# Kernel tuning notes

Hardware: AMD Instinct MI355X
Metric: run time of the kernel (lower is better)

The kernel has to match this reference:

```python
import jax, jax.numpy as jnp
import numpy as np

N_NODES = 50000
N_EDGES = 800000
D_IN = 64
D_OUT = 64


def setup_inputs() -> dict:
    key = jax.random.key(0)
    k1, k2, k3 = jax.random.split(key, 3)
    x = jax.random.normal(k1, (N_NODES, D_IN), dtype=jnp.float32)
    edge_index = jax.random.randint(k2, (2, N_EDGES), 0, N_NODES, dtype=jnp.int64)
    # xavier_uniform for weight [in, out]
    limit = np.sqrt(6.0 / (D_IN + D_OUT)).astype(np.float32)
    weight = jax.random.uniform(k3, (D_IN, D_OUT), dtype=jnp.float32, minval=-limit, maxval=limit)
    bias = jnp.zeros((D_OUT,), dtype=jnp.float32)
    return {"x": x, "edge_index": edge_index, "weight": weight, "bias": bias}


def reference(x, edge_index, weight, bias):
    n = x.shape[0]
    # add self loops
    loops = jnp.arange(n, dtype=edge_index.dtype)
    row = jnp.concatenate([edge_index[0], loops])  # [E+N]
    col = jnp.concatenate([edge_index[1], loops])  # [E+N]
    # degree over row (as in torch_geometric degree(row, N))
    deg = jax.ops.segment_sum(jnp.ones_like(row, dtype=x.dtype), row, num_segments=n)
    deg_inv_sqrt = jnp.where(deg > 0, jax.lax.rsqrt(deg), jnp.zeros_like(deg))
    norm = deg_inv_sqrt[row] * deg_inv_sqrt[col]  # [E+N]
    h = x @ weight  # [N, D_OUT]
    # gather-scale-scatter: out[col] += h[row] * norm
    out = jax.ops.segment_sum(h[row] * norm[:, None], col, num_segments=n)
    return out + bias
```

## Files before the change

kernel.cpp:

```cpp
#include <hip/hip_runtime.h>
#include <hip/hip_bf16.h>


constexpr int N_NODES = 50000;
constexpr int N_EDGES = 800000;
constexpr int D = 64;
constexpr int NB_SCAN = (N_NODES + 255) / 256;

constexpr int B_SLICE = 64;
constexpr int SLICE = N_EDGES / B_SLICE;
constexpr int PACK8 = N_NODES / 4;
constexpr int QUAR = N_NODES / 4;

static __device__ __forceinline__ unsigned short f2bf(float f) {
    unsigned u = __float_as_uint(f);
    unsigned r = (u + 0x7fffu + ((u >> 16) & 1u)) >> 16;
    return (unsigned short)r;
}
static __device__ __forceinline__ float bf2f(unsigned short s) {
    return __uint_as_float((unsigned)s << 16);
}

__global__ __launch_bounds__(1024) void hist_priv_kernel(const int* __restrict__ ei,
                                                         unsigned* __restrict__ bh) {
    __shared__ unsigned loc[PACK8];
    int b = blockIdx.x;
    int s = b & (B_SLICE - 1);
    const int* arr = (b < B_SLICE) ? ei : ei + N_EDGES;
    for (int w = threadIdx.x; w < PACK8; w += 1024) loc[w] = 0;
    __syncthreads();
    const int* p = arr + s * SLICE;
    for (int i = threadIdx.x; i < SLICE; i += 1024) {
        int k = p[i];
        atomicAdd(&loc[k >> 2], 1u << (8 * (k & 3)));
    }
    __syncthreads();
    unsigned* dst = bh + (size_t)b * PACK8;
    for (int w = threadIdx.x; w < PACK8; w += 1024) dst[w] = loc[w];
}

__global__ __launch_bounds__(256) void reduce_scan_kernel(const unsigned* __restrict__ bh,
                                                          float* __restrict__ dis,
                                                          int* __restrict__ offs_local,
                                                          int* __restrict__ partials,
                                                          unsigned char* __restrict__ bs8) {
    int t = threadIdx.x;
    int i = blockIdx.x * 256 + t;
    unsigned cl = 0;
    if (i < N_NODES) {
        const int w = i >> 2;
        const unsigned sh = 8 * (i & 3);
        const unsigned* prow = bh + w;
        unsigned dl = 0;
#pragma unroll
        for (int g = 0; g < 4; ++g) {
            unsigned vr[16];
#pragma unroll
            for (int k = 0; k < 16; ++k) vr[k] = prow[(size_t)(g * 16 + k) * PACK8];
#pragma unroll
            for (int k = 0; k < 16; ++k) dl += (vr[k] >> sh) & 0xffu;
        }
        dis[i] = rsqrtf((float)dl + 1.0f);
        const unsigned* pcol = bh + (size_t)B_SLICE * PACK8 + w;
#pragma unroll
        for (int g = 0; g < 4; ++g) {
            unsigned vr[16];
#pragma unroll
            for (int k = 0; k < 16; ++k) vr[k] = pcol[(size_t)(g * 16 + k) * PACK8];
#pragma unroll
            for (int k = 0; k < 16; ++k) {
                bs8[(size_t)(g * 16 + k) * N_NODES + i] = (unsigned char)cl;
                cl += (vr[k] >> sh) & 0xffu;
            }
        }
    }
    __shared__ int s[256];
    s[t] = (int)cl;
    __syncthreads();
    for (int d = 1; d < 256; d <<= 1) {
        int u = (t >= d) ? s[t - d] : 0;
        __syncthreads();
        s[t] += u;
        __syncthreads();
    }
    if (i < N_NODES) offs_local[i] = s[t] - (int)cl;
    if (t == 255) partials[blockIdx.x] = s[t];
}

__global__ __launch_bounds__(256, 4) void gemm_kernel(const float* __restrict__ x,
                                                      const float* __restrict__ W,
                                                      const float* __restrict__ dis,
                                                      unsigned short* __restrict__ hs) {
    __shared__ float Xs[64][68];
    __shared__ float Ws[64][64];
    int t = threadIdx.x;
    int n0 = blockIdx.x * 64;

    const float4* W4 = (const float4*)W;
    float4* Ws4 = (float4*)Ws;
#pragma unroll
    for (int i = 0; i < 4; ++i) Ws4[t + i * 256] = W4[t + i * 256];

    const float4* x4 = (const float4*)(x + (size_t)n0 * D);
#pragma unroll
    for (int i = 0; i < 4; ++i) {
        int f = t + i * 256;
        int r = f >> 4, c = (f & 15) << 2;
        float4 v = make_float4(0.f, 0.f, 0.f, 0.f);
        if (n0 + r < N_NODES) v = x4[f];
        Xs[r][c] = v.x; Xs[r][c + 1] = v.y; Xs[r][c + 2] = v.z; Xs[r][c + 3] = v.w;
    }
    __syncthreads();

    int tx = t & 15, ty = t >> 4;
    float acc[4][4] = {};
#pragma unroll 8
    for (int k = 0; k < D; ++k) {
        float a[4], bb[4];
#pragma unroll
        for (int i = 0; i < 4; ++i) a[i] = Xs[ty * 4 + i][k];
#pragma unroll
        for (int jj = 0; jj < 4; ++jj) bb[jj] = Ws[k][tx * 4 + jj];
#pragma unroll
        for (int i = 0; i < 4; ++i)
#pragma unroll
            for (int jj = 0; jj < 4; ++jj)
                acc[i][jj] = fmaf(a[i], bb[jj], acc[i][jj]);
    }

#pragma unroll
    for (int i = 0; i < 4; ++i) {
        int r = ty * 4 + i;
        if (n0 + r < N_NODES) {
            float dr = dis[n0 + r];
            ushort4 v;
            v.x = f2bf(acc[i][0] * dr); v.y = f2bf(acc[i][1] * dr);
            v.z = f2bf(acc[i][2] * dr); v.w = f2bf(acc[i][3] * dr);
            *(ushort4*)(hs + (size_t)(n0 + r) * D + tx * 4) = v;
        }
    }
}

__global__ __launch_bounds__(1024) void bucket_det_kernel(const int* __restrict__ ei,
                                                          const int* __restrict__ offs_local,
                                                          const int* __restrict__ partials,
                                                          const unsigned char* __restrict__ bs8,
                                                          int* __restrict__ csr,
                                                          int* __restrict__ offs) {
    __shared__ unsigned pos[QUAR];
    __shared__ int pref[256];
    const int t = threadIdx.x;

    if (t < 256) pref[t] = (t < NB_SCAN) ? partials[t] : 0;
    __syncthreads();
    for (int d = 1; d < 256; d <<= 1) {
        int u = 0;
        if (t < 256 && t >= d) u = pref[t - d];
        __syncthreads();
        if (t < 256) pref[t] += u;
        __syncthreads();
    }
    if (t < 256) {
        int inc = pref[t];
        int own = (t < NB_SCAN) ? partials[t] : 0;
        pref[t] = inc - own;
    }
    __syncthreads();

    const int s = blockIdx.x >> 2;
    const int q = blockIdx.x & 3;
    const int c0 = q * QUAR;
    const int* olq = offs_local + c0;
    const unsigned char* relq = bs8 + (size_t)s * N_NODES + c0;
    const bool write_offs = (s == 0);
    for (int w = t; w < QUAR; w += 1024) {
        int node = c0 + w;
        int off = pref[node >> 8] + olq[w];
        pos[w] = (unsigned)off + relq[w];
        if (write_offs) offs[node] = off;
    }
    if (write_offs && q == 3 && t == 0) offs[N_NODES] = N_EDGES;
    __syncthreads();

    const int* rowp = ei + s * SLICE;
    const int* colp = ei + N_EDGES + s * SLICE;
    for (int i = t; i < SLICE; i += 1024) {
        int c = colp[i];
        if (c >= c0 && c < c0 + QUAR) {
            unsigned p = atomicAdd(&pos[c - c0], 1u);
            csr[p] = rowp[i];
        }
    }
}

__global__ __launch_bounds__(256) void gather_kernel(const int* __restrict__ offs,
                                                     const int* __restrict__ csr,
                                                     const unsigned short* __restrict__ hs,
                                                     const float* __restrict__ dis,
                                                     const float* __restrict__ bias,
                                                     float* __restrict__ out) {
    int wave = threadIdx.x >> 6;
    int j = threadIdx.x & 63;
    int n = blockIdx.x * 4 + wave;
    if (n >= N_NODES) return;

    float a[8];
    a[0] = bf2f(hs[(size_t)n * D + j]);
#pragma unroll
    for (int k = 1; k < 8; ++k) a[k] = 0.f;

    int beg = __builtin_amdgcn_readfirstlane(offs[n]);
    int m   = __builtin_amdgcn_readfirstlane(offs[n + 1]) - beg;
    const int* p = csr + beg;

    int i = 0;
    for (; i + 16 <= m; i += 16) {
        int r[16];
        float v[16];
#pragma unroll
        for (int k = 0; k < 16; ++k) r[k] = p[i + k];
#pragma unroll
        for (int k = 0; k < 16; ++k) v[k] = bf2f(hs[(size_t)r[k] * D + j]);
#pragma unroll
        for (int k = 0; k < 16; ++k) a[k & 7] += v[k];
    }
    for (; i + 4 <= m; i += 4) {
        int r0 = p[i], r1 = p[i + 1], r2 = p[i + 2], r3 = p[i + 3];
        a[0] += bf2f(hs[(size_t)r0 * D + j]);
        a[1] += bf2f(hs[(size_t)r1 * D + j]);
        a[2] += bf2f(hs[(size_t)r2 * D + j]);
        a[3] += bf2f(hs[(size_t)r3 * D + j]);
    }
    for (; i < m; ++i) a[1] += bf2f(hs[(size_t)p[i] * D + j]);
    float tot = ((a[0] + a[1]) + (a[2] + a[3])) + ((a[4] + a[5]) + (a[6] + a[7]));
    out[(size_t)n * D + j] = fmaf(dis[n], tot, bias[j]);
}


__global__ void histf_kernel(const int* __restrict__ row, const int* __restrict__ col,
                             int* __restrict__ degi, int* __restrict__ cnt) {
    int e = blockIdx.x * blockDim.x + threadIdx.x;
    if (e < N_EDGES) {
        atomicAdd(&degi[row[e]], 1);
        atomicAdd(&cnt[col[e]], 1);
    }
}

__global__ void disf_kernel(int* __restrict__ degi) {
    int i = blockIdx.x * blockDim.x + threadIdx.x;
    if (i < N_NODES) {
        float d = (float)degi[i] + 1.0f;
        ((float*)degi)[i] = rsqrtf(d);
    }
}

__global__ void block_scan_kernel(const int* __restrict__ cnt, int* __restrict__ offs,
                                  int* __restrict__ partials) {
    __shared__ int s[256];
    int t = threadIdx.x;
    int i = blockIdx.x * 256 + t;
    int v = (i < N_NODES) ? cnt[i] : 0;
    s[t] = v;
    __syncthreads();
    for (int d = 1; d < 256; d <<= 1) {
        int u = (t >= d) ? s[t - d] : 0;
        __syncthreads();
        s[t] += u;
        __syncthreads();
    }
    if (i < N_NODES) offs[i] = s[t] - v;
    if (t == 255) partials[blockIdx.x] = s[t];
}

__global__ void scan_partials_kernel(int* __restrict__ partials) {
    __shared__ int s[256];
    int t = threadIdx.x;
    int v = (t < NB_SCAN) ? partials[t] : 0;
    s[t] = v;
    __syncthreads();
    for (int d = 1; d < 256; d <<= 1) {
        int u = (t >= d) ? s[t - d] : 0;
        __syncthreads();
        s[t] += u;
        __syncthreads();
    }
    if (t < NB_SCAN) partials[t] = s[t] - v;
}

__global__ void add_off_kernel(int* __restrict__ offs, const int* __restrict__ partials) {
    int i = blockIdx.x * 256 + threadIdx.x;
    if (i < N_NODES) offs[i] += partials[blockIdx.x];
    if (i == 0) offs[N_NODES] = N_EDGES;
}

__global__ void bucket_fb_kernel(const int* __restrict__ row, const int* __restrict__ col,
                                 const int* __restrict__ offs, int* __restrict__ cur,
                                 int* __restrict__ csr) {
    int e = blockIdx.x * blockDim.x + threadIdx.x;
    if (e < N_EDGES) {
        int c = col[e];
        int pos = offs[c] + atomicAdd(&cur[c], 1);
        csr[pos] = row[e];
    }
}


extern "C" void kernel_launch(void* const* d_in, const int* in_sizes, int n_in,
                              void* d_out, int out_size, void* d_ws, size_t ws_size,
                              hipStream_t stream) {
    const float* x    = (const float*)d_in[0];
    const int*   ei   = (const int*)d_in[1];
    const float* W    = (const float*)d_in[2];
    const float* bias = (const float*)d_in[3];
    float* out = (float*)d_out;

    char* ws = (char*)d_ws;
    float*          dis      = (float*)(ws + 0);
    int*            offs     = (int*)(ws + 200000);
    int*            offs_loc = (int*)(ws + 400064);
    int*            cur      = (int*)(ws + 600064);
    int*            partials = (int*)(ws + 800064);
    int*            csr      = (int*)(ws + 801088);
    unsigned short* hs       = (unsigned short*)(ws + 4001088);
    unsigned*       bh       = (unsigned*)(ws + 10401088);
    unsigned char*  bs8      = (unsigned char*)(ws + 16801088);

    const size_t WS_NEEDED = 20001088;

    if (ws_size >= WS_NEEDED) {
        hist_priv_kernel<<<2 * B_SLICE, 1024, 0, stream>>>(ei, bh);
        reduce_scan_kernel<<<NB_SCAN, 256, 0, stream>>>(bh, dis, offs_loc, partials, bs8);
        gemm_kernel<<<(N_NODES + 63) / 64, 256, 0, stream>>>(x, W, dis, hs);
        bucket_det_kernel<<<4 * B_SLICE, 1024, 0, stream>>>(ei, offs_loc, partials, bs8,
                                                            csr, offs);
        gather_kernel<<<(N_NODES + 3) / 4, 256, 0, stream>>>(offs, csr, hs, dis, bias, out);
    } else {
        const int* row = ei;
        const int* col = ei + N_EDGES;
        int* degi = (int*)dis;
        int* cntf = offs_loc;
        hipMemsetAsync(ws, 0, 800064, stream);
        histf_kernel<<<(N_EDGES + 255) / 256, 256, 0, stream>>>(row, col, degi, cntf);
        disf_kernel<<<(N_NODES + 255) / 256, 256, 0, stream>>>(degi);
        block_scan_kernel<<<NB_SCAN, 256, 0, stream>>>(cntf, offs, partials);
        scan_partials_kernel<<<1, 256, 0, stream>>>(partials);
        add_off_kernel<<<NB_SCAN, 256, 0, stream>>>(offs, partials);
        gemm_kernel<<<(N_NODES + 63) / 64, 256, 0, stream>>>(x, W, dis, hs);
        bucket_fb_kernel<<<(N_EDGES + 255) / 256, 256, 0, stream>>>(row, col, offs, cur, csr);
        gather_kernel<<<(N_NODES + 3) / 4, 256, 0, stream>>>(offs, csr, hs, dis, bias, out);
    }
}
```

Baseline: 134.1 us.

## Move offset computation into GEMM and pack bucket cursors as bytes in LDS

The global CSR offset computation (scan of block partials plus local offsets) moves out of every bucket block and into the first blocks of the GEMM kernel, which writes offs to global memory. The bucket kernel then initializes its shared cursors from per-slice byte-relative counts packed four per 32-bit word and uses shifted atomic adds, cutting its LDS footprint by 4x and dropping the redundant per-block scan. Each edge now reads offs[c] from global memory. Correctness relies on per-slice per-node counts staying below 256 so byte counters never overflow into neighbours.

```diff
diff --git a/kernel.cpp b/kernel.cpp
--- a/kernel.cpp
+++ b/kernel.cpp
@@ -90,10 +90,32 @@
 __global__ __launch_bounds__(256, 4) void gemm_kernel(const float* __restrict__ x,
                                                       const float* __restrict__ W,
                                                       const float* __restrict__ dis,
-                                                      unsigned short* __restrict__ hs) {
+                                                      unsigned short* __restrict__ hs,
+                                                      const int* __restrict__ offs_local,
+                                                      const int* __restrict__ partials,
+                                                      int* __restrict__ offs,
+                                                      int do_offs) {
     __shared__ float Xs[64][68];
     __shared__ float Ws[64][64];
+    __shared__ int pref[256];
     int t = threadIdx.x;
+    int b = blockIdx.x;
+
+    if (do_offs && b < NB_SCAN) {
+        pref[t] = (t < NB_SCAN) ? partials[t] : 0;
+        __syncthreads();
+        for (int d = 1; d < 256; d <<= 1) {
+            int u = (t >= d) ? pref[t - d] : 0;
+            __syncthreads();
+            pref[t] += u;
+            __syncthreads();
+        }
+        int base = pref[b] - partials[b];
+        int node = b * 256 + t;
+        if (node < N_NODES) offs[node] = base + offs_local[node];
+        if (b == 0 && t == 0) offs[N_NODES] = N_EDGES;
+    }
+
     int n0 = blockIdx.x * 64;
 
     const float4* W4 = (const float4*)W;
@@ -142,53 +164,29 @@
 }
 
 __global__ __launch_bounds__(1024) void bucket_det_kernel(const int* __restrict__ ei,
-                                                          const int* __restrict__ offs_local,
-                                                          const int* __restrict__ partials,
                                                           const unsigned char* __restrict__ bs8,
-                                                          int* __restrict__ csr,
-                                                          int* __restrict__ offs) {
-    __shared__ unsigned pos[QUAR];
-    __shared__ int pref[256];
+                                                          const int* __restrict__ offs,
+                                                          int* __restrict__ csr) {
+    __shared__ unsigned pos[QUAR / 4];
     const int t = threadIdx.x;
-
-    if (t < 256) pref[t] = (t < NB_SCAN) ? partials[t] : 0;
-    __syncthreads();
-    for (int d = 1; d < 256; d <<= 1) {
-        int u = 0;
-        if (t < 256 && t >= d) u = pref[t - d];
-        __syncthreads();
-        if (t < 256) pref[t] += u;
-        __syncthreads();
-    }
-    if (t < 256) {
-        int inc = pref[t];
-        int own = (t < NB_SCAN) ? partials[t] : 0;
-        pref[t] = inc - own;
-    }
-    __syncthreads();
-
     const int s = blockIdx.x >> 2;
     const int q = blockIdx.x & 3;
     const int c0 = q * QUAR;
-    const int* olq = offs_local + c0;
-    const unsigned char* relq = bs8 + (size_t)s * N_NODES + c0;
-    const bool write_offs = (s == 0);
-    for (int w = t; w < QUAR; w += 1024) {
-        int node = c0 + w;
-        int off = pref[node >> 8] + olq[w];
-        pos[w] = (unsigned)off + relq[w];
-        if (write_offs) offs[node] = off;
-    }
-    if (write_offs && q == 3 && t == 0) offs[N_NODES] = N_EDGES;
+
+    const unsigned* rel32 = (const unsigned*)(bs8 + (size_t)s * N_NODES + c0);
+    for (int w = t; w < QUAR / 4; w += 1024) pos[w] = rel32[w];
     __syncthreads();
 
     const int* rowp = ei + s * SLICE;
     const int* colp = ei + N_EDGES + s * SLICE;
     for (int i = t; i < SLICE; i += 1024) {
         int c = colp[i];
-        if (c >= c0 && c < c0 + QUAR) {
-            unsigned p = atomicAdd(&pos[c - c0], 1u);
-            csr[p] = rowp[i];
+        unsigned cc = (unsigned)(c - c0);
+        if (cc < (unsigned)QUAR) {
+            int base = offs[c];
+            unsigned old = atomicAdd(&pos[cc >> 2], 1u << (8 * (cc & 3)));
+            unsigned rel = (old >> (8 * (cc & 3))) & 0xffu;
+            csr[base + (int)rel] = rowp[i];
         }
     }
 }
@@ -330,9 +328,9 @@
     if (ws_size >= WS_NEEDED) {
         hist_priv_kernel<<<2 * B_SLICE, 1024, 0, stream>>>(ei, bh);
         reduce_scan_kernel<<<NB_SCAN, 256, 0, stream>>>(bh, dis, offs_loc, partials, bs8);
-        gemm_kernel<<<(N_NODES + 63) / 64, 256, 0, stream>>>(x, W, dis, hs);
-        bucket_det_kernel<<<4 * B_SLICE, 1024, 0, stream>>>(ei, offs_loc, partials, bs8,
-                                                            csr, offs);
+        gemm_kernel<<<(N_NODES + 63) / 64, 256, 0, stream>>>(x, W, dis, hs,
+                                                             offs_loc, partials, offs, 1);
+        bucket_det_kernel<<<4 * B_SLICE, 1024, 0, stream>>>(ei, bs8, offs, csr);
         gather_kernel<<<(N_NODES + 3) / 4, 256, 0, stream>>>(offs, csr, hs, dis, bias, out);
     } else {
         const int* row = ei;
@@ -345,7 +343,8 @@
         block_scan_kernel<<<NB_SCAN, 256, 0, stream>>>(cntf, offs, partials);
         scan_partials_kernel<<<1, 256, 0, stream>>>(partials);
         add_off_kernel<<<NB_SCAN, 256, 0, stream>>>(offs, partials);
-        gemm_kernel<<<(N_NODES + 63) / 64, 256, 0, stream>>>(x, W, dis, hs);
+        gemm_kernel<<<(N_NODES + 63) / 64, 256, 0, stream>>>(x, W, dis, hs,
+                                                             offs_loc, partials, offs, 0);
         bucket_fb_kernel<<<(N_EDGES + 255) / 256, 256, 0, stream>>>(row, col, offs, cur, csr);
         gather_kernel<<<(N_NODES + 3) / 4, 256, 0, stream>>>(offs, csr, hs, dis, bias, out);
     }
```

Result: faster. 128.7 us (-4.0%).

## Fuse histogram with GEMM kernel, move source-degree scaling into gather

Applied to the files above, without the earlier changes.

Removes the GEMM's dependence on the degree array by applying the source-node rsqrt-degree scale inside the gather loop instead. This lets the GEMM run in the same launch as the private-histogram kernel, with the two block types sharing one LDS buffer. The bucket kernel now keeps packed 8-bit per-node counters in LDS instead of full 32-bit positions, cutting its LDS footprint and init work, and computes each edge's base offset on the fly. In exchange the gather does an extra dis[] load per edge, and the fused kernel needs a large LDS allocation that may limit occupancy.

```diff
diff --git a/kernel.cpp b/kernel.cpp
--- a/kernel.cpp
+++ b/kernel.cpp
@@ -11,6 +11,7 @@
 constexpr int SLICE = N_EDGES / B_SLICE;
 constexpr int PACK8 = N_NODES / 4;
 constexpr int QUAR = N_NODES / 4;
+constexpr int NB_GEMM = (N_NODES / 64 + 1 + 3) / 4;
 
 static __device__ __forceinline__ unsigned short f2bf(float f) {
     unsigned u = __float_as_uint(f);
@@ -21,22 +22,82 @@
     return __uint_as_float((unsigned)s << 16);
 }
 
-__global__ __launch_bounds__(1024) void hist_priv_kernel(const int* __restrict__ ei,
-                                                         unsigned* __restrict__ bh) {
-    __shared__ unsigned loc[PACK8];
-    int b = blockIdx.x;
-    int s = b & (B_SLICE - 1);
-    const int* arr = (b < B_SLICE) ? ei : ei + N_EDGES;
-    for (int w = threadIdx.x; w < PACK8; w += 1024) loc[w] = 0;
-    __syncthreads();
-    const int* p = arr + s * SLICE;
-    for (int i = threadIdx.x; i < SLICE; i += 1024) {
-        int k = p[i];
-        atomicAdd(&loc[k >> 2], 1u << (8 * (k & 3)));
-    }
-    __syncthreads();
-    unsigned* dst = bh + (size_t)b * PACK8;
-    for (int w = threadIdx.x; w < PACK8; w += 1024) dst[w] = loc[w];
+struct GemmLds {
+    float Ws[64][64];
+    float Xs[4][64][68];
+};
+constexpr size_t HIST_LDS = (size_t)PACK8 * 4;
+constexpr size_t FUSED_LDS = sizeof(GemmLds) > HIST_LDS ? sizeof(GemmLds) : HIST_LDS;
+
+__global__ __launch_bounds__(1024, 4) void fused_hist_gemm(
+        const int* __restrict__ ei, unsigned* __restrict__ bh,
+        const float* __restrict__ x, const float* __restrict__ W,
+        unsigned short* __restrict__ hs) {
+    __shared__ __align__(16) char ldsraw[FUSED_LDS];
+    const int b = blockIdx.x;
+    const int t = threadIdx.x;
+
+    if (b < 2 * B_SLICE) {
+        unsigned* loc = (unsigned*)ldsraw;
+        int s = b & (B_SLICE - 1);
+        const int* arr = (b < B_SLICE) ? ei : ei + N_EDGES;
+        for (int w = t; w < PACK8; w += 1024) loc[w] = 0;
+        __syncthreads();
+        const int* p = arr + s * SLICE;
+        for (int i = t; i < SLICE; i += 1024) {
+            int k = p[i];
+            atomicAdd(&loc[k >> 2], 1u << (8 * (k & 3)));
+        }
+        __syncthreads();
+        unsigned* dst = bh + (size_t)b * PACK8;
+        for (int w = t; w < PACK8; w += 1024) dst[w] = loc[w];
+    } else {
+        GemmLds* g = (GemmLds*)ldsraw;
+        const int grp = t >> 8, t256 = t & 255;
+        const int tb = (b - 2 * B_SLICE) * 4 + grp;
+        const int n0 = tb * 64;
+
+        ((float4*)g->Ws)[t] = ((const float4*)W)[t];
+
+        float (*Xs)[68] = g->Xs[grp];
+        const float4* x4 = (const float4*)(x + (size_t)n0 * D);
+#pragma unroll
+        for (int i = 0; i < 4; ++i) {
+            int f = t256 + i * 256;
+            int r = f >> 4, c = (f & 15) << 2;
+            float4 v = make_float4(0.f, 0.f, 0.f, 0.f);
+            if (n0 + r < N_NODES) v = x4[f];
+            Xs[r][c] = v.x; Xs[r][c + 1] = v.y; Xs[r][c + 2] = v.z; Xs[r][c + 3] = v.w;
+        }
+        __syncthreads();
+
+        int tx = t256 & 15, ty = t256 >> 4;
+        float acc[4][4] = {};
+#pragma unroll 8
+        for (int k = 0; k < D; ++k) {
+            float a[4], bb[4];
+#pragma unroll
+            for (int i = 0; i < 4; ++i) a[i] = Xs[ty * 4 + i][k];
+#pragma unroll
+            for (int jj = 0; jj < 4; ++jj) bb[jj] = g->Ws[k][tx * 4 + jj];
+#pragma unroll
+            for (int i = 0; i < 4; ++i)
+#pragma unroll
+                for (int jj = 0; jj < 4; ++jj)
+                    acc[i][jj] = fmaf(a[i], bb[jj], acc[i][jj]);
+        }
+
+#pragma unroll
+        for (int i = 0; i < 4; ++i) {
+            int r = ty * 4 + i;
+            if (n0 + r < N_NODES) {
+                ushort4 v;
+                v.x = f2bf(acc[i][0]); v.y = f2bf(acc[i][1]);
+                v.z = f2bf(acc[i][2]); v.w = f2bf(acc[i][3]);
+                *(ushort4*)(hs + (size_t)(n0 + r) * D + tx * 4) = v;
+            }
+        }
+    }
 }
 
 __global__ __launch_bounds__(256) void reduce_scan_kernel(const unsigned* __restrict__ bh,
@@ -87,67 +148,13 @@
     if (t == 255) partials[blockIdx.x] = s[t];
 }
 
-__global__ __launch_bounds__(256, 4) void gemm_kernel(const float* __restrict__ x,
-                                                      const float* __restrict__ W,
-                                                      const float* __restrict__ dis,
-                                                      unsigned short* __restrict__ hs) {
-    __shared__ float Xs[64][68];
-    __shared__ float Ws[64][64];
-    int t = threadIdx.x;
-    int n0 = blockIdx.x * 64;
-
-    const float4* W4 = (const float4*)W;
-    float4* Ws4 = (float4*)Ws;
-#pragma unroll
-    for (int i = 0; i < 4; ++i) Ws4[t + i * 256] = W4[t + i * 256];
-
-    const float4* x4 = (const float4*)(x + (size_t)n0 * D);
-#pragma unroll
-    for (int i = 0; i < 4; ++i) {
-        int f = t + i * 256;
-        int r = f >> 4, c = (f & 15) << 2;
-        float4 v = make_float4(0.f, 0.f, 0.f, 0.f);
-        if (n0 + r < N_NODES) v = x4[f];
-        Xs[r][c] = v.x; Xs[r][c + 1] = v.y; Xs[r][c + 2] = v.z; Xs[r][c + 3] = v.w;
-    }
-    __syncthreads();
-
-    int tx = t & 15, ty = t >> 4;
-    float acc[4][4] = {};
-#pragma unroll 8
-    for (int k = 0; k < D; ++k) {
-        float a[4], bb[4];
-#pragma unroll
-        for (int i = 0; i < 4; ++i) a[i] = Xs[ty * 4 + i][k];
-#pragma unroll
-        for (int jj = 0; jj < 4; ++jj) bb[jj] = Ws[k][tx * 4 + jj];
-#pragma unroll
-        for (int i = 0; i < 4; ++i)
-#pragma unroll
-            for (int jj = 0; jj < 4; ++jj)
-                acc[i][jj] = fmaf(a[i], bb[jj], acc[i][jj]);
-    }
-
-#pragma unroll
-    for (int i = 0; i < 4; ++i) {
-        int r = ty * 4 + i;
-        if (n0 + r < N_NODES) {
-            float dr = dis[n0 + r];
-            ushort4 v;
-            v.x = f2bf(acc[i][0] * dr); v.y = f2bf(acc[i][1] * dr);
-            v.z = f2bf(acc[i][2] * dr); v.w = f2bf(acc[i][3] * dr);
-            *(ushort4*)(hs + (size_t)(n0 + r) * D + tx * 4) = v;
-        }
-    }
-}
-
 __global__ __launch_bounds__(1024) void bucket_det_kernel(const int* __restrict__ ei,
                                                           const int* __restrict__ offs_local,
                                                           const int* __restrict__ partials,
                                                           const unsigned char* __restrict__ bs8,
                                                           int* __restrict__ csr,
                                                           int* __restrict__ offs) {
-    __shared__ unsigned pos[QUAR];
+    __shared__ unsigned pos[QUAR / 4];
     __shared__ int pref[256];
     const int t = threadIdx.x;
 
@@ -170,25 +177,30 @@
     const int s = blockIdx.x >> 2;
     const int q = blockIdx.x & 3;
     const int c0 = q * QUAR;
-    const int* olq = offs_local + c0;
-    const unsigned char* relq = bs8 + (size_t)s * N_NODES + c0;
-    const bool write_offs = (s == 0);
-    for (int w = t; w < QUAR; w += 1024) {
-        int node = c0 + w;
-        int off = pref[node >> 8] + olq[w];
-        pos[w] = (unsigned)off + relq[w];
-        if (write_offs) offs[node] = off;
-    }
-    if (write_offs && q == 3 && t == 0) offs[N_NODES] = N_EDGES;
+
+    const unsigned* rel32 = (const unsigned*)(bs8 + (size_t)s * N_NODES + c0);
+    for (int w = t; w < QUAR / 4; w += 1024) pos[w] = rel32[w];
+
+    if (s == 0) {
+        const int* olq = offs_local + c0;
+        for (int w = t; w < QUAR; w += 1024) {
+            int node = c0 + w;
+            offs[node] = pref[node >> 8] + olq[w];
+        }
+        if (q == 3 && t == 0) offs[N_NODES] = N_EDGES;
+    }
     __syncthreads();
 
     const int* rowp = ei + s * SLICE;
     const int* colp = ei + N_EDGES + s * SLICE;
     for (int i = t; i < SLICE; i += 1024) {
         int c = colp[i];
-        if (c >= c0 && c < c0 + QUAR) {
-            unsigned p = atomicAdd(&pos[c - c0], 1u);
-            csr[p] = rowp[i];
+        unsigned cc = (unsigned)(c - c0);
+        if (cc < (unsigned)QUAR) {
+            int base = pref[c >> 8] + offs_local[c];
+            unsigned old = atomicAdd(&pos[cc >> 2], 1u << (8 * (cc & 3)));
+            unsigned rel = (old >> (8 * (cc & 3))) & 0xffu;
+            csr[base + (int)rel] = rowp[i];
         }
     }
 }
@@ -204,8 +216,9 @@
     int n = blockIdx.x * 4 + wave;
     if (n >= N_NODES) return;
 
+    float dn = dis[n];
     float a[8];
-    a[0] = bf2f(hs[(size_t)n * D + j]);
+    a[0] = dn * bf2f(hs[(size_t)n * D + j]);
 #pragma unroll
     for (int k = 1; k < 8; ++k) a[k] = 0.f;
 
@@ -216,26 +229,84 @@
     int i = 0;
     for (; i + 16 <= m; i += 16) {
         int r[16];
+        float dr[16];
         float v[16];
 #pragma unroll
         for (int k = 0; k < 16; ++k) r[k] = p[i + k];
 #pragma unroll
+        for (int k = 0; k < 16; ++k) dr[k] = dis[r[k]];
+#pragma unroll
         for (int k = 0; k < 16; ++k) v[k] = bf2f(hs[(size_t)r[k] * D + j]);
 #pragma unroll
-        for (int k = 0; k < 16; ++k) a[k & 7] += v[k];
+        for (int k = 0; k < 16; ++k) a[k & 7] = fmaf(v[k], dr[k], a[k & 7]);
     }
     for (; i + 4 <= m; i += 4) {
         int r0 = p[i], r1 = p[i + 1], r2 = p[i + 2], r3 = p[i + 3];
-        a[0] += bf2f(hs[(size_t)r0 * D + j]);
-        a[1] += bf2f(hs[(size_t)r1 * D + j]);
-        a[2] += bf2f(hs[(size_t)r2 * D + j]);
-        a[3] += bf2f(hs[(size_t)r3 * D + j]);
-    }
-    for (; i < m; ++i) a[1] += bf2f(hs[(size_t)p[i] * D + j]);
+        a[0] = fmaf(bf2f(hs[(size_t)r0 * D + j]), dis[r0], a[0]);
+        a[1] = fmaf(bf2f(hs[(size_t)r1 * D + j]), dis[r1], a[1]);
+        a[2] = fmaf(bf2f(hs[(size_t)r2 * D + j]), dis[r2], a[2]);
+        a[3] = fmaf(bf2f(hs[(size_t)r3 * D + j]), dis[r3], a[3]);
+    }
+    for (; i < m; ++i) {
+        int r0 = p[i];
+        a[1] = fmaf(bf2f(hs[(size_t)r0 * D + j]), dis[r0], a[1]);
+    }
     float tot = ((a[0] + a[1]) + (a[2] + a[3])) + ((a[4] + a[5]) + (a[6] + a[7]));
-    out[(size_t)n * D + j] = fmaf(dis[n], tot, bias[j]);
-}
-
+    out[(size_t)n * D + j] = fmaf(dn, tot, bias[j]);
+}
+
+
+__global__ __launch_bounds__(256, 4) void gemm_plain_kernel(const float* __restrict__ x,
+                                                            const float* __restrict__ W,
+                                                            unsigned short* __restrict__ hs) {
+    __shared__ float Xs[64][68];
+    __shared__ float Ws[64][64];
+    int t = threadIdx.x;
+    int n0 = blockIdx.x * 64;
+
+    const float4* W4 = (const float4*)W;
+    float4* Ws4 = (float4*)Ws;
+#pragma unroll
+    for (int i = 0; i < 4; ++i) Ws4[t + i * 256] = W4[t + i * 256];
+
+    const float4* x4 = (const float4*)(x + (size_t)n0 * D);
+#pragma unroll
+    for (int i = 0; i < 4; ++i) {
+        int f = t + i * 256;
+        int r = f >> 4, c = (f & 15) << 2;
+        float4 v = make_float4(0.f, 0.f, 0.f, 0.f);
+        if (n0 + r < N_NODES) v = x4[f];
+        Xs[r][c] = v.x; Xs[r][c + 1] = v.y; Xs[r][c + 2] = v.z; Xs[r][c + 3] = v.w;
+    }
+    __syncthreads();
+
+    int tx = t & 15, ty = t >> 4;
+    float acc[4][4] = {};
+#pragma unroll 8
+    for (int k = 0; k < D; ++k) {
+        float a[4], bb[4];
+#pragma unroll
+        for (int i = 0; i < 4; ++i) a[i] = Xs[ty * 4 + i][k];
+#pragma unroll
+        for (int jj = 0; jj < 4; ++jj) bb[jj] = Ws[k][tx * 4 + jj];
+#pragma unroll
+        for (int i = 0; i < 4; ++i)
+#pragma unroll
+            for (int jj = 0; jj < 4; ++jj)
+                acc[i][jj] = fmaf(a[i], bb[jj], acc[i][jj]);
+    }
+
+#pragma unroll
+    for (int i = 0; i < 4; ++i) {
+        int r = ty * 4 + i;
+        if (n0 + r < N_NODES) {
+            ushort4 v;
+            v.x = f2bf(acc[i][0]); v.y = f2bf(acc[i][1]);
+            v.z = f2bf(acc[i][2]); v.w = f2bf(acc[i][3]);
+            *(ushort4*)(hs + (size_t)(n0 + r) * D + tx * 4) = v;
+        }
+    }
+}
 
 __global__ void histf_kernel(const int* __restrict__ row, const int* __restrict__ col,
                              int* __restrict__ degi, int* __restrict__ cnt) {
@@ -328,9 +399,8 @@
     const size_t WS_NEEDED = 20001088;
 
     if (ws_size >= WS_NEEDED) {
-        hist_priv_kernel<<<2 * B_SLICE, 1024, 0, stream>>>(ei, bh);
+        fused_hist_gemm<<<2 * B_SLICE + NB_GEMM, 1024, 0, stream>>>(ei, bh, x, W, hs);
         reduce_scan_kernel<<<NB_SCAN, 256, 0, stream>>>(bh, dis, offs_loc, partials, bs8);
-        gemm_kernel<<<(N_NODES + 63) / 64, 256, 0, stream>>>(x, W, dis, hs);
         bucket_det_kernel<<<4 * B_SLICE, 1024, 0, stream>>>(ei, offs_loc, partials, bs8,
                                                             csr, offs);
         gather_kernel<<<(N_NODES + 3) / 4, 256, 0, stream>>>(offs, csr, hs, dis, bias, out);
@@ -345,7 +415,7 @@
         block_scan_kernel<<<NB_SCAN, 256, 0, stream>>>(cntf, offs, partials);
         scan_partials_kernel<<<1, 256, 0, stream>>>(partials);
         add_off_kernel<<<NB_SCAN, 256, 0, stream>>>(offs, partials);
-        gemm_kernel<<<(N_NODES + 63) / 64, 256, 0, stream>>>(x, W, dis, hs);
+        gemm_plain_kernel<<<(N_NODES + 63) / 64, 256, 0, stream>>>(x, W, hs);
         bucket_fb_kernel<<<(N_EDGES + 255) / 256, 256, 0, stream>>>(row, col, offs, cur, csr);
         gather_kernel<<<(N_NODES + 3) / 4, 256, 0, stream>>>(offs, csr, hs, dis, bias, out);
     }
```

Result: no change. 135.0 us (+0.7%).
